# Kernel optimization log

Measured on AMD Instinct MI355X. Metric: run time of the kernel, lower is better.

The kernel has to match this reference:

```python
import jax, jax.numpy as jnp
import numpy as np

TAU = 0.5
EPS = 1e-12  # torch F.normalize default eps


def _l2norm(x):
    n = jnp.sqrt(jnp.sum(x * x, axis=1, keepdims=True))
    return x / jnp.maximum(n, EPS)


def _semi_loss(z1, z2, tau):
    z1n = _l2norm(z1)
    z2n = _l2norm(z2)
    refl = jnp.exp(jnp.matmul(z1n, z1n.T) / tau)      # [N, N]
    between = jnp.exp(jnp.matmul(z1n, z2n.T) / tau)   # [N, N]
    num = jnp.diagonal(between)
    den = refl.sum(axis=1) + between.sum(axis=1) - jnp.diagonal(refl)
    return -jnp.mean(jnp.log(num / den))


def setup_inputs() -> dict:
    key = jax.random.key(0)
    k1, k2 = jax.random.split(key)
    N, D = 8192, 256
    H_1 = jax.random.normal(k1, (N, D), dtype=jnp.float32)
    H_2 = jax.random.normal(k2, (N, D), dtype=jnp.float32)
    return {"H_1": H_1, "H_2": H_2}


def reference(H_1, H_2):
    l1 = _semi_loss(H_1, H_2, TAU)
    l2 = _semi_loss(H_2, H_1, TAU)
    return (l1 + l2) * 0.5
```

## Files before the change

kernel.cpp:

```cpp
#include <hip/hip_runtime.h>
#include <math.h>

#define NROW 8192
#define DDIM 256
#define BM 128
#define BN 64
#define BK 128
#define NT_SYM 2080
#define NT_FULL 4096
#define NT_TOTAL (2 * NT_SYM + NT_FULL)
#define GRID (2 * NT_TOTAL)

typedef __attribute__((ext_vector_type(16))) float f32x16;
typedef __attribute__((ext_vector_type(4)))  int   i32x4;
typedef __attribute__((ext_vector_type(8)))  int   i32x8;
typedef __attribute__((address_space(3))) unsigned int lds_u32;
typedef const __attribute__((address_space(1))) unsigned int glb_u32;

template <int CTRL>
static __device__ inline float dpp_ror_add(float v) {
    int s = __float_as_int(v);
    int r = __builtin_amdgcn_update_dpp(0, s, CTRL, 0xF, 0xF, true);
    return v + __int_as_float(r);
}
static __device__ inline float row16_sum(float v) {
    v = dpp_ror_add<0x121>(v);
    v = dpp_ror_add<0x122>(v);
    v = dpp_ror_add<0x124>(v);
    v = dpp_ror_add<0x128>(v);
    return v;
}

static __device__ inline unsigned int pack_fp8x4(float a, float b, float c, float d) {
    int p = __builtin_amdgcn_cvt_pk_fp8_f32(a, b, 0, false);
    p = __builtin_amdgcn_cvt_pk_fp8_f32(c, d, p, true);
    return (unsigned int)p;
}

__global__ __launch_bounds__(256) void normalize_kernel(
        const float* __restrict__ h1, const float* __restrict__ h2,
        unsigned char* __restrict__ z1b, unsigned char* __restrict__ z2b,
        float* __restrict__ diag,
        float* __restrict__ rs1, float* __restrict__ rs2,
        float* __restrict__ rbr, float* __restrict__ rbc,
        float* __restrict__ out) {
    int wave = threadIdx.x >> 6;
    int lane = threadIdx.x & 63;
    int row  = blockIdx.x * 4 + wave;
    if (blockIdx.x == 0 && threadIdx.x == 0) out[0] = 0.f;
    const float4* p1 = (const float4*)(h1 + (size_t)row * DDIM);
    const float4* p2 = (const float4*)(h2 + (size_t)row * DDIM);
    float4 a = p1[lane];
    float4 b = p2[lane];
    float s1 = a.x*a.x + a.y*a.y + a.z*a.z + a.w*a.w;
    float s2 = b.x*b.x + b.y*b.y + b.z*b.z + b.w*b.w;
    #pragma unroll
    for (int m = 1; m < 64; m <<= 1) { s1 += __shfl_xor(s1, m); s2 += __shfl_xor(s2, m); }
    float r1 = 1.0f / fmaxf(sqrtf(s1), 1e-12f);
    float r2 = 1.0f / fmaxf(sqrtf(s2), 1e-12f);
    float n1x = a.x*r1, n1y = a.y*r1, n1z = a.z*r1, n1w = a.w*r1;
    float n2x = b.x*r2, n2y = b.y*r2, n2z = b.z*r2, n2w = b.w*r2;
    float dt = n1x*n2x + n1y*n2y + n1z*n2z + n1w*n2w;
    #pragma unroll
    for (int m = 1; m < 64; m <<= 1) dt += __shfl_xor(dt, m);
    if (lane == 0) {
        diag[row] = 2.0f * dt;
        rs1[row] = 0.f; rs2[row] = 0.f; rbr[row] = 0.f; rbc[row] = 0.f;
    }
    const float SC = 1.69864364f;
    ((unsigned int*)(z1b + (size_t)row * DDIM))[lane] =
        pack_fp8x4(n1x*SC, n1y*SC, n1z*SC, n1w*SC);
    ((unsigned int*)(z2b + (size_t)row * DDIM))[lane] =
        pack_fp8x4(n2x*SC, n2y*SC, n2z*SC, n2w*SC);
}

__global__ __launch_bounds__(256, 6) void expsum_kernel(
        const unsigned char* __restrict__ z1, const unsigned char* __restrict__ z2,
        float* __restrict__ rs1, float* __restrict__ rs2,
        float* __restrict__ rbr, float* __restrict__ rbc) {
    int t  = blockIdx.x >> 1;
    int ch = blockIdx.x & 1;
    int kind, tt;
    if (t < NT_SYM)            { kind = 0; tt = t; }
    else if (t < 2 * NT_SYM)   { kind = 1; tt = t - NT_SYM; }
    else                       { kind = 2; tt = t - 2 * NT_SYM; }

    int by, bx;
    const unsigned char *Ap, *Bp;
    float *rowsum, *colsum;
    if (kind == 2) {
        by = tt >> 6; bx = tt & 63;
        Ap = z1; Bp = z2; rowsum = rbr; colsum = rbc;
    } else {
        by = (int)((sqrtf(8.0f * (float)tt + 1.0f) - 1.0f) * 0.5f);
        while ((by + 1) * (by + 2) / 2 <= tt) ++by;
        while (by * (by + 1) / 2 > tt) --by;
        bx = tt - by * (by + 1) / 2;
        const unsigned char* z = (kind == 0) ? z1 : z2;
        Ap = z; Bp = z;
        rowsum = (kind == 0) ? rs1 : rs2;
        colsum = (bx == by) ? nullptr : rowsum;
    }

    const int rt = by * BM;
    const int ct = bx * BM + ch * BN;

    __shared__ __align__(16) unsigned char lA[BM * BK];
    __shared__ __align__(16) unsigned char lB[BN * BK];
    __shared__ float lds_rp[2][BM];
    __shared__ float lds_cp[2][BN];

    const int tid  = threadIdx.x;
    const int lane = tid & 63;
    const int wid  = tid >> 6;
    const int wr   = wid & 1;
    const int wc   = wid >> 1;
    const int l31  = lane & 31;
    const int kh   = lane >> 5;

    const int srow = lane >> 3;
    const int sgt  = lane & 7;

    const int sw16 = (l31 & 7);

    const int aoff0 = (wr * 64 + l31) * BK;
    const int aoff1 = aoff0 + 32 * BK;
    const int boff  = (wc * 32 + l31) * BK;

    const unsigned char* gA[4];
    lds_u32* ldA[4];
    #pragma unroll
    for (int p = 0; p < 4; ++p) {
        int r0 = (p * 4 + wid) * 8;
        int r  = r0 + srow;
        int gg = sgt ^ (r & 7);
        gA[p]  = Ap + (size_t)(rt + r) * DDIM + gg * 16;
        ldA[p] = (lds_u32*)(lA + r0 * BK);
    }
    const unsigned char* gB[2];
    lds_u32* ldB[2];
    #pragma unroll
    for (int p = 0; p < 2; ++p) {
        int r0 = (p * 4 + wid) * 8;
        int r  = r0 + srow;
        int gg = sgt ^ (r & 7);
        gB[p]  = Bp + (size_t)(ct + r) * DDIM + gg * 16;
        ldB[p] = (lds_u32*)(lB + r0 * BK);
    }

    f32x16 acc0, acc1;
    #pragma unroll
    for (int r = 0; r < 16; ++r) { acc0[r] = 0.f; acc1[r] = 0.f; }

    #pragma unroll
    for (int kt = 0; kt < 2; ++kt) {
        if (kt == 0) {
            #pragma unroll
            for (int p = 0; p < 4; ++p)
                __builtin_amdgcn_global_load_lds((glb_u32*)gA[p], ldA[p], 16, 0, 0);
            #pragma unroll
            for (int p = 0; p < 2; ++p)
                __builtin_amdgcn_global_load_lds((glb_u32*)gB[p], ldB[p], 16, 0, 0);
        } else {
            #pragma unroll
            for (int p = 0; p < 4; ++p)
                __builtin_amdgcn_global_load_lds((glb_u32*)gA[p], ldA[p], 16, 128, 0);
            #pragma unroll
            for (int p = 0; p < 2; ++p)
                __builtin_amdgcn_global_load_lds((glb_u32*)gB[p], ldB[p], 16, 128, 0);
        }
        __syncthreads();
        #pragma unroll
        for (int ks = 0; ks < 2; ++ks) {
            const int g0   = ks * 4 + kh * 2;
            const int off0 = (g0 ^ sw16) * 16;
            const int off1 = off0 ^ 16;
            i32x8 a0, a1, bv;
            *((i32x4*)&a0)     = *(const i32x4*)(lA + aoff0 + off0);
            *((i32x4*)&a0 + 1) = *(const i32x4*)(lA + aoff0 + off1);
            *((i32x4*)&a1)     = *(const i32x4*)(lA + aoff1 + off0);
            *((i32x4*)&a1 + 1) = *(const i32x4*)(lA + aoff1 + off1);
            *((i32x4*)&bv)     = *(const i32x4*)(lB + boff  + off0);
            *((i32x4*)&bv + 1) = *(const i32x4*)(lB + boff  + off1);
            acc0 = __builtin_amdgcn_mfma_scale_f32_32x32x64_f8f6f4(
                a0, bv, acc0, 0, 0, 0, 0x7F7F7F7F, 0, 0x7F7F7F7F);
            acc1 = __builtin_amdgcn_mfma_scale_f32_32x32x64_f8f6f4(
                a1, bv, acc1, 0, 0, 0, 0x7F7F7F7F, 0, 0x7F7F7F7F);
        }
        __syncthreads();
    }

    float colpart = 0.f;
    #pragma unroll
    for (int r = 0; r < 16; ++r) {
        float e0 = __builtin_amdgcn_exp2f(acc0[r]);
        float e1 = __builtin_amdgcn_exp2f(acc1[r]);
        colpart += e0 + e1;
        float v0 = row16_sum(e0);
        v0 += __shfl_xor(v0, 16);
        float v1 = row16_sum(e1);
        v1 += __shfl_xor(v1, 16);
        if (l31 == 0) {
            int rloc = wr * 64 + 4 * kh + (r & 3) + 8 * (r >> 2);
            lds_rp[wc][rloc]      = v0;
            lds_rp[wc][rloc + 32] = v1;
        }
    }
    float cp = colpart + __shfl_xor(colpart, 32);
    if (lane < 32) lds_cp[wr][wc * 32 + l31] = cp;
    __syncthreads();
    if (tid < BM) {
        atomicAdd(&rowsum[rt + tid], lds_rp[0][tid] + lds_rp[1][tid]);
    } else if (colsum && tid < BM + BN) {
        int c = tid - BM;
        atomicAdd(&colsum[ct + c], lds_cp[0][c] + lds_cp[1][c]);
    }
}

__global__ __launch_bounds__(256) void finalize_kernel(
        const float* __restrict__ rs1, const float* __restrict__ rs2,
        const float* __restrict__ rbr, const float* __restrict__ rbc,
        const float* __restrict__ diag, float* __restrict__ out) {
    __shared__ float s4[4];
    const float E2 = 7.38905609893065f;
    int i = blockIdx.x * 256 + threadIdx.x;
    float den1 = rs1[i] + rbr[i] - E2;
    float den2 = rs2[i] + rbc[i] - E2;
    float v = 0.5f * (logf(den1) + logf(den2)) - diag[i];
    #pragma unroll
    for (int m = 1; m < 64; m <<= 1) v += __shfl_xor(v, m);
    if ((threadIdx.x & 63) == 0) s4[threadIdx.x >> 6] = v;
    __syncthreads();
    if (threadIdx.x == 0) {
        float t = (s4[0] + s4[1] + s4[2] + s4[3]) * (1.0f / (float)NROW);
        atomicAdd(out, t);
    }
}

extern "C" void kernel_launch(void* const* d_in, const int* in_sizes, int n_in,
                              void* d_out, int out_size, void* d_ws, size_t ws_size,
                              hipStream_t stream) {
    const float* h1 = (const float*)d_in[0];
    const float* h2 = (const float*)d_in[1];
    float* out = (float*)d_out;

    char* ws = (char*)d_ws;
    unsigned char* z1b = (unsigned char*)ws;
    unsigned char* z2b = (unsigned char*)(ws + (size_t)NROW * DDIM);
    float* sums = (float*)(ws + (size_t)2 * NROW * DDIM);
    float* rs1  = sums;
    float* rs2  = sums + NROW;
    float* rbr  = sums + 2 * NROW;
    float* rbc  = sums + 3 * NROW;
    float* diag = sums + 4 * NROW;

    normalize_kernel<<<NROW / 4, 256, 0, stream>>>(h1, h2, z1b, z2b, diag,
                                                   rs1, rs2, rbr, rbc, out);

    expsum_kernel<<<GRID, 256, 0, stream>>>(z1b, z2b, rs1, rs2, rbr, rbc);

    finalize_kernel<<<NROW / 256, 256, 0, stream>>>(rs1, rs2, rbr, rbc, diag, out);
}
```

Measured before the change: 148.0 us.

## Load B operand directly from global into registers, bypassing LDS

The B tile is no longer staged through LDS. Each lane loads its B fragment straight from global memory into registers, so the B LDS buffer and its reads are removed. The epilogue also drops the cross-lane shuffle reductions and writes partial row and column sums into a larger LDS array, which are summed before the atomics. This cuts LDS traffic and footprint, but the per-lane global loads may be less coalesced and their latency is exposed before the barrier.

```diff
diff --git a/kernel.cpp b/kernel.cpp
--- a/kernel.cpp
+++ b/kernel.cpp
@@ -106,9 +106,8 @@
     const int ct = bx * BM + ch * BN;
 
     __shared__ __align__(16) unsigned char lA[BM * BK];
-    __shared__ __align__(16) unsigned char lB[BN * BK];
-    __shared__ float lds_rp[2][BM];
-    __shared__ float lds_cp[2][BN];
+    __shared__ float lds_rp[2][2][BM];
+    __shared__ float lds_cp[2][2][BN];
 
     const int tid  = threadIdx.x;
     const int lane = tid & 63;
@@ -125,7 +124,6 @@
 
     const int aoff0 = (wr * 64 + l31) * BK;
     const int aoff1 = aoff0 + 32 * BK;
-    const int boff  = (wc * 32 + l31) * BK;
 
     const unsigned char* gA[4];
     lds_u32* ldA[4];
@@ -137,16 +135,8 @@
         gA[p]  = Ap + (size_t)(rt + r) * DDIM + gg * 16;
         ldA[p] = (lds_u32*)(lA + r0 * BK);
     }
-    const unsigned char* gB[2];
-    lds_u32* ldB[2];
-    #pragma unroll
-    for (int p = 0; p < 2; ++p) {
-        int r0 = (p * 4 + wid) * 8;
-        int r  = r0 + srow;
-        int gg = sgt ^ (r & 7);
-        gB[p]  = Bp + (size_t)(ct + r) * DDIM + gg * 16;
-        ldB[p] = (lds_u32*)(lB + r0 * BK);
-    }
+    const unsigned char* gBbase =
+        Bp + (size_t)(ct + wc * 32 + l31) * DDIM + kh * 32;
 
     f32x16 acc0, acc1;
     #pragma unroll
@@ -158,30 +148,28 @@
             #pragma unroll
             for (int p = 0; p < 4; ++p)
                 __builtin_amdgcn_global_load_lds((glb_u32*)gA[p], ldA[p], 16, 0, 0);
-            #pragma unroll
-            for (int p = 0; p < 2; ++p)
-                __builtin_amdgcn_global_load_lds((glb_u32*)gB[p], ldB[p], 16, 0, 0);
         } else {
             #pragma unroll
             for (int p = 0; p < 4; ++p)
                 __builtin_amdgcn_global_load_lds((glb_u32*)gA[p], ldA[p], 16, 128, 0);
-            #pragma unroll
-            for (int p = 0; p < 2; ++p)
-                __builtin_amdgcn_global_load_lds((glb_u32*)gB[p], ldB[p], 16, 128, 0);
         }
+        i32x8 bv0, bv1;
+        *((i32x4*)&bv0)     = *(const i32x4*)(gBbase + kt * 128);
+        *((i32x4*)&bv0 + 1) = *(const i32x4*)(gBbase + kt * 128 + 16);
+        *((i32x4*)&bv1)     = *(const i32x4*)(gBbase + kt * 128 + 64);
+        *((i32x4*)&bv1 + 1) = *(const i32x4*)(gBbase + kt * 128 + 80);
         __syncthreads();
         #pragma unroll
         for (int ks = 0; ks < 2; ++ks) {
             const int g0   = ks * 4 + kh * 2;
             const int off0 = (g0 ^ sw16) * 16;
             const int off1 = off0 ^ 16;
-            i32x8 a0, a1, bv;
+            i32x8 a0, a1;
             *((i32x4*)&a0)     = *(const i32x4*)(lA + aoff0 + off0);
             *((i32x4*)&a0 + 1) = *(const i32x4*)(lA + aoff0 + off1);
             *((i32x4*)&a1)     = *(const i32x4*)(lA + aoff1 + off0);
             *((i32x4*)&a1 + 1) = *(const i32x4*)(lA + aoff1 + off1);
-            *((i32x4*)&bv)     = *(const i32x4*)(lB + boff  + off0);
-            *((i32x4*)&bv + 1) = *(const i32x4*)(lB + boff  + off1);
+            const i32x8 bv = (ks == 0) ? bv0 : bv1;
             acc0 = __builtin_amdgcn_mfma_scale_f32_32x32x64_f8f6f4(
                 a0, bv, acc0, 0, 0, 0, 0x7F7F7F7F, 0, 0x7F7F7F7F);
             acc1 = __builtin_amdgcn_mfma_scale_f32_32x32x64_f8f6f4(
@@ -190,30 +178,33 @@
         __syncthreads();
     }
 
-    float colpart = 0.f;
+    float cp0 = 0.f, cp1 = 0.f;
     #pragma unroll
     for (int r = 0; r < 16; ++r) {
         float e0 = __builtin_amdgcn_exp2f(acc0[r]);
         float e1 = __builtin_amdgcn_exp2f(acc1[r]);
-        colpart += e0 + e1;
+        cp0 += e0;
+        cp1 += e1;
         float v0 = row16_sum(e0);
-        v0 += __shfl_xor(v0, 16);
         float v1 = row16_sum(e1);
-        v1 += __shfl_xor(v1, 16);
-        if (l31 == 0) {
+        if ((lane & 15) == 0) {
             int rloc = wr * 64 + 4 * kh + (r & 3) + 8 * (r >> 2);
-            lds_rp[wc][rloc]      = v0;
-            lds_rp[wc][rloc + 32] = v1;
+            int colhalf = l31 >> 4;
+            lds_rp[wc][colhalf][rloc]      = v0;
+            lds_rp[wc][colhalf][rloc + 32] = v1;
         }
     }
-    float cp = colpart + __shfl_xor(colpart, 32);
-    if (lane < 32) lds_cp[wr][wc * 32 + l31] = cp;
+    lds_cp[wr][kh][wc * 32 + l31] = cp0 + cp1;
     __syncthreads();
     if (tid < BM) {
-        atomicAdd(&rowsum[rt + tid], lds_rp[0][tid] + lds_rp[1][tid]);
+        float s = lds_rp[0][0][tid] + lds_rp[0][1][tid]
+                + lds_rp[1][0][tid] + lds_rp[1][1][tid];
+        atomicAdd(&rowsum[rt + tid], s);
     } else if (colsum && tid < BM + BN) {
         int c = tid - BM;
-        atomicAdd(&colsum[ct + c], lds_cp[0][c] + lds_cp[1][c]);
+        float s = lds_cp[0][0][c] + lds_cp[0][1][c]
+                + lds_cp[1][0][c] + lds_cp[1][1][c];
+        atomicAdd(&colsum[ct + c], s);
     }
 }
 
```

New measurement: 147.5 us. No clear change (-0.3%).
